# Kernel optimization log

Measured on AMD Instinct MI355X. Metric: run time of the kernel, lower is better.

The kernel has to match this reference:

```python
import jax, jax.numpy as jnp
import numpy as np

B, S, V, D = 64, 1024, 1024, 512


def setup_inputs() -> dict:
    key = jax.random.key(0)
    ks = jax.random.split(key, 18)
    sd = 1.0 / np.sqrt(D)
    return dict(
        map_memory=jnp.zeros((B, S, V), jnp.float32),
        step_memory=jnp.zeros((B, S, S), jnp.float32),
        evidence=jax.random.normal(ks[0], (B, D), jnp.float32),
        marker_id=jax.random.randint(ks[1], (B,), 0, 4, jnp.int32),
        source_idx=jax.random.randint(ks[2], (B,), 0, S, jnp.int32),
        source_mask=jax.random.randint(ks[3], (B,), 0, 2, jnp.int32).astype(bool),
        target_symbol_idx=jax.random.randint(ks[4], (B,), 0, S, jnp.int32),
        target_symbol_mask=jax.random.randint(ks[5], (B,), 0, 2, jnp.int32).astype(bool),
        target_value_idx=jax.random.randint(ks[6], (B,), 0, V, jnp.int32),
        target_value_mask=jax.random.randint(ks[7], (B,), 0, 2, jnp.int32).astype(bool),
        map_W1=jax.random.normal(ks[8], (D, D), jnp.float32) * sd,
        map_b1=jnp.zeros((D,), jnp.float32),
        map_W2=jax.random.normal(ks[9], (D, 1), jnp.float32) * sd,
        map_b2=jnp.zeros((1,), jnp.float32),
        step_W1=jax.random.normal(ks[10], (D, D), jnp.float32) * sd,
        step_b1=jnp.zeros((D,), jnp.float32),
        step_W2=jax.random.normal(ks[11], (D, 1), jnp.float32) * sd,
        step_b2=jnp.zeros((1,), jnp.float32),
    )


def _gain(x, W1, b1, W2, b2):
    # Dense -> gelu (flax default: approximate) -> Dense(1)
    h = jax.nn.gelu(x @ W1 + b1)
    return (h @ W2 + b2)[:, 0]  # [B]


def reference(map_memory, step_memory, evidence, marker_id, source_idx,
              source_mask, target_symbol_idx, target_symbol_mask,
              target_value_idx, target_value_mask,
              map_W1, map_b1, map_W2, map_b2,
              step_W1, step_b1, step_W2, step_b2):
    map_gate = jax.nn.sigmoid(_gain(evidence, map_W1, map_b1, map_W2, map_b2))    # [B]
    step_gate = jax.nn.sigmoid(_gain(evidence, step_W1, step_b1, step_W2, step_b2))  # [B]
    map_mask = ((marker_id == 1) | (marker_id == 2)) & source_mask & target_value_mask
    step_mask = (marker_id == 3) & source_mask & target_symbol_mask
    b = jnp.arange(map_memory.shape[0])
    # one-hot outer product 'bs,bv->bsv' * gate is exactly a single gated entry at
    # (source_idx, target_idx) per batch element -> indexed scatter-add.
    next_map = map_memory.at[b, source_idx, target_value_idx].add(
        map_gate * map_mask.astype(map_gate.dtype))
    next_step = step_memory.at[b, source_idx, target_symbol_idx].add(
        step_gate * step_mask.astype(step_gate.dtype))
    return next_map, next_step
```

## Files before the change

### kernel.cpp

```cpp
#include <hip/hip_runtime.h>
#include <math.h>

#define BB 64
#define SS 1024
#define VV 1024
#define DD 512

__device__ __forceinline__ float gelu_tanh(float x) {
    const float k = 0.7978845608028654f;
    float x3 = x * x * x;
    return 0.5f * x * (1.0f + tanhf(k * (x + 0.044715f * x3)));
}

__global__ void __launch_bounds__(256)
gate_scatter_kernel(
    const float* __restrict__ evidence,
    const int* __restrict__ marker_id,
    const int* __restrict__ source_idx,
    const int* __restrict__ source_mask,
    const int* __restrict__ target_symbol_idx,
    const int* __restrict__ target_symbol_mask,
    const int* __restrict__ target_value_idx,
    const int* __restrict__ target_value_mask,
    const float* __restrict__ map_W1, const float* __restrict__ map_b1,
    const float* __restrict__ map_W2, const float* __restrict__ map_b2,
    const float* __restrict__ step_W1, const float* __restrict__ step_b1,
    const float* __restrict__ step_W2, const float* __restrict__ step_b2,
    float* __restrict__ out)
{
    const int b    = blockIdx.x >> 1;
    const int head = blockIdx.x & 1;
    const float* W1  = head ? step_W1 : map_W1;
    const float* b1  = head ? step_b1 : map_b1;
    const float* W2  = head ? step_W2 : map_W2;
    const float* b2v = head ? step_b2 : map_b2;

    __shared__ float ev[DD];
    __shared__ float wsum[4];

    const int tid = threadIdx.x;
    for (int i = tid; i < DD; i += 256) ev[i] = evidence[b * DD + i];
    __syncthreads();

    float acc = 0.0f;
    #pragma unroll
    for (int jj = 0; jj < DD; jj += 256) {
        const int j = jj + tid;
        float h = b1[j];
        for (int k = 0; k < DD; ++k) {
            h = fmaf(ev[k], W1[k * DD + j], h);
        }
        h = gelu_tanh(h);
        acc = fmaf(h, W2[j], acc);
    }

    #pragma unroll
    for (int off = 32; off > 0; off >>= 1) acc += __shfl_down(acc, off, 64);
    if ((tid & 63) == 0) wsum[tid >> 6] = acc;
    __syncthreads();

    if (tid == 0) {
        float g = wsum[0] + wsum[1] + wsum[2] + wsum[3] + b2v[0];
        g = 1.0f / (1.0f + expf(-g));
        const int m  = marker_id[b];
        const bool sm = source_mask[b] != 0;
        if (head == 0) {
            const bool mask = ((m == 1) || (m == 2)) && sm && (target_value_mask[b] != 0);
            if (mask) {
                size_t idx = (size_t)b * SS * VV + (size_t)source_idx[b] * VV
                           + (size_t)target_value_idx[b];
                out[idx] += g;
            }
        } else {
            const bool mask = (m == 3) && sm && (target_symbol_mask[b] != 0);
            if (mask) {
                size_t idx = (size_t)BB * SS * VV + (size_t)b * SS * SS
                           + (size_t)source_idx[b] * SS + (size_t)target_symbol_idx[b];
                out[idx] += g;
            }
        }
    }
}

extern "C" void kernel_launch(void* const* d_in, const int* in_sizes, int n_in,
                              void* d_out, int out_size, void* d_ws, size_t ws_size,
                              hipStream_t stream) {
    const float* map_memory  = (const float*)d_in[0];
    const float* step_memory = (const float*)d_in[1];
    const float* evidence    = (const float*)d_in[2];
    const int* marker_id     = (const int*)d_in[3];
    const int* source_idx    = (const int*)d_in[4];
    const int* source_mask         = (const int*)d_in[5];
    const int* target_symbol_idx   = (const int*)d_in[6];
    const int* target_symbol_mask  = (const int*)d_in[7];
    const int* target_value_idx    = (const int*)d_in[8];
    const int* target_value_mask   = (const int*)d_in[9];
    const float* map_W1  = (const float*)d_in[10];
    const float* map_b1  = (const float*)d_in[11];
    const float* map_W2  = (const float*)d_in[12];
    const float* map_b2  = (const float*)d_in[13];
    const float* step_W1 = (const float*)d_in[14];
    const float* step_b1 = (const float*)d_in[15];
    const float* step_W2 = (const float*)d_in[16];
    const float* step_b2 = (const float*)d_in[17];

    float* out = (float*)d_out;
    const size_t map_elems  = (size_t)BB * SS * VV;
    const size_t step_elems = (size_t)BB * SS * SS;

    hipMemcpyAsync(out, map_memory, map_elems * sizeof(float),
                   hipMemcpyDeviceToDevice, stream);
    hipMemcpyAsync(out + map_elems, step_memory, step_elems * sizeof(float),
                   hipMemcpyDeviceToDevice, stream);

    dim3 grid(BB * 2);
    dim3 block(256);
    gate_scatter_kernel<<<grid, block, 0, stream>>>(
        evidence, marker_id, source_idx, source_mask,
        target_symbol_idx, target_symbol_mask,
        target_value_idx, target_value_mask,
        map_W1, map_b1, map_W2, map_b2,
        step_W1, step_b1, step_W2, step_b2,
        out);
}
```

Baseline: 246.7 us.

## Fuse memory copy with gated scatter into a single vectorized copy kernel

Replaces the two device-to-device memcpys and the separate scatter kernel with a gate kernel that writes scatter indices and gate values to workspace, followed by a float4 copy kernel that applies matching updates while streaming the memory. This removes the read-modify-write tail and the memcpy launch overhead, and lets the copy be a custom kernel. It adds an extra pass over the index list in every copy block, and the int indices stay close to the 32-bit range.

Result: slower. 253.0 us (+2.5%).

```diff
diff --git a/kernel.cpp b/kernel.cpp
--- a/kernel.cpp
+++ b/kernel.cpp
@@ -6,6 +6,15 @@
 #define VV 1024
 #define DD 512
 
+#define MAP_WORDS  ((size_t)BB * SS * VV)
+#define STEP_WORDS ((size_t)BB * SS * SS)
+#define TOT_WORDS  (MAP_WORDS + STEP_WORDS)
+#define TOT_F4     (TOT_WORDS / 4)
+#define MAP_F4     (MAP_WORDS / 4)
+#define COPY_BLOCKS 8192
+#define F4_PER_BLOCK (TOT_F4 / COPY_BLOCKS)
+#define NGATES (BB * 2)
+
 __device__ __forceinline__ float gelu_tanh(float x) {
     const float k = 0.7978845608028654f;
     float x3 = x * x * x;
@@ -13,7 +22,7 @@
 }
 
 __global__ void __launch_bounds__(256)
-gate_scatter_kernel(
+gate_kernel(
     const float* __restrict__ evidence,
     const int* __restrict__ marker_id,
     const int* __restrict__ source_idx,
@@ -26,7 +35,7 @@
     const float* __restrict__ map_W2, const float* __restrict__ map_b2,
     const float* __restrict__ step_W1, const float* __restrict__ step_b1,
     const float* __restrict__ step_W2, const float* __restrict__ step_b2,
-    float* __restrict__ out)
+    int* __restrict__ ws_idx, float* __restrict__ ws_g)
 {
     const int b    = blockIdx.x >> 1;
     const int head = blockIdx.x & 1;
@@ -64,21 +73,75 @@
         g = 1.0f / (1.0f + expf(-g));
         const int m  = marker_id[b];
         const bool sm = source_mask[b] != 0;
+        int idx = -1;
         if (head == 0) {
-            const bool mask = ((m == 1) || (m == 2)) && sm && (target_value_mask[b] != 0);
-            if (mask) {
-                size_t idx = (size_t)b * SS * VV + (size_t)source_idx[b] * VV
-                           + (size_t)target_value_idx[b];
-                out[idx] += g;
+            if (((m == 1) || (m == 2)) && sm && (target_value_mask[b] != 0)) {
+                idx = b * (SS * VV) + source_idx[b] * VV + target_value_idx[b];
             }
         } else {
-            const bool mask = (m == 3) && sm && (target_symbol_mask[b] != 0);
-            if (mask) {
-                size_t idx = (size_t)BB * SS * VV + (size_t)b * SS * SS
-                           + (size_t)source_idx[b] * SS + (size_t)target_symbol_idx[b];
-                out[idx] += g;
+            if ((m == 3) && sm && (target_symbol_mask[b] != 0)) {
+                idx = (int)MAP_WORDS + b * (SS * SS) + source_idx[b] * SS
+                    + target_symbol_idx[b];
             }
         }
+        ws_idx[blockIdx.x] = idx;
+        ws_g[blockIdx.x]   = g;
+    }
+}
+
+__global__ void __launch_bounds__(256)
+copy_scatter_kernel(
+    const float4* __restrict__ map_memory,
+    const float4* __restrict__ step_memory,
+    const int* __restrict__ ws_idx,
+    const float* __restrict__ ws_g,
+    float4* __restrict__ out)
+{
+    const long f4_base = (long)blockIdx.x * F4_PER_BLOCK;
+
+    __shared__ int n_match;
+    __shared__ int m_f4[8];
+    __shared__ int m_lane[8];
+    __shared__ float m_g[8];
+
+    if (threadIdx.x == 0) n_match = 0;
+    __syncthreads();
+    if (threadIdx.x < NGATES) {
+        int idx = ws_idx[threadIdx.x];
+        if (idx >= 0) {
+            long f4 = (long)(idx >> 2);
+            long off = f4 - f4_base;
+            if (off >= 0 && off < F4_PER_BLOCK) {
+                int slot = atomicAdd(&n_match, 1);
+                m_f4[slot]   = (int)off;
+                m_lane[slot] = idx & 3;
+                m_g[slot]    = ws_g[threadIdx.x];
+            }
+        }
+    }
+    __syncthreads();
+    const int nm = n_match;
+
+    const float4* __restrict__ src =
+        (f4_base < (long)MAP_F4) ? (map_memory + f4_base)
+                                 : (step_memory + (f4_base - (long)MAP_F4));
+    float4* __restrict__ dst = out + f4_base;
+
+    for (int i = threadIdx.x; i < F4_PER_BLOCK; i += 256) {
+        float4 v = src[i];
+        if (nm) {
+            for (int e = 0; e < nm; ++e) {
+                if (m_f4[e] == i) {
+                    const int ln = m_lane[e];
+                    const float g = m_g[e];
+                    v.x += (ln == 0) ? g : 0.0f;
+                    v.y += (ln == 1) ? g : 0.0f;
+                    v.z += (ln == 2) ? g : 0.0f;
+                    v.w += (ln == 3) ? g : 0.0f;
+                }
+            }
+        }
+        dst[i] = v;
     }
 }
 
@@ -90,11 +153,11 @@
     const float* evidence    = (const float*)d_in[2];
     const int* marker_id     = (const int*)d_in[3];
     const int* source_idx    = (const int*)d_in[4];
-    const int* source_mask         = (const int*)d_in[5];
-    const int* target_symbol_idx   = (const int*)d_in[6];
-    const int* target_symbol_mask  = (const int*)d_in[7];
-    const int* target_value_idx    = (const int*)d_in[8];
-    const int* target_value_mask   = (const int*)d_in[9];
+    const int* source_mask        = (const int*)d_in[5];
+    const int* target_symbol_idx  = (const int*)d_in[6];
+    const int* target_symbol_mask = (const int*)d_in[7];
+    const int* target_value_idx   = (const int*)d_in[8];
+    const int* target_value_mask  = (const int*)d_in[9];
     const float* map_W1  = (const float*)d_in[10];
     const float* map_b1  = (const float*)d_in[11];
     const float* map_W2  = (const float*)d_in[12];
@@ -104,22 +167,19 @@
     const float* step_W2 = (const float*)d_in[16];
     const float* step_b2 = (const float*)d_in[17];
 
-    float* out = (float*)d_out;
-    const size_t map_elems  = (size_t)BB * SS * VV;
-    const size_t step_elems = (size_t)BB * SS * SS;
+    char* ws = (char*)d_ws;
+    int*   ws_idx = (int*)ws;
+    float* ws_g   = (float*)(ws + NGATES * sizeof(int));
 
-    hipMemcpyAsync(out, map_memory, map_elems * sizeof(float),
-                   hipMemcpyDeviceToDevice, stream);
-    hipMemcpyAsync(out + map_elems, step_memory, step_elems * sizeof(float),
-                   hipMemcpyDeviceToDevice, stream);
-
-    dim3 grid(BB * 2);
-    dim3 block(256);
-    gate_scatter_kernel<<<grid, block, 0, stream>>>(
+    gate_kernel<<<dim3(NGATES), dim3(256), 0, stream>>>(
         evidence, marker_id, source_idx, source_mask,
         target_symbol_idx, target_symbol_mask,
         target_value_idx, target_value_mask,
         map_W1, map_b1, map_W2, map_b2,
         step_W1, step_b1, step_W2, step_b2,
-        out);
+        ws_idx, ws_g);
+
+    copy_scatter_kernel<<<dim3(COPY_BLOCKS), dim3(256), 0, stream>>>(
+        (const float4*)map_memory, (const float4*)step_memory,
+        ws_idx, ws_g, (float4*)d_out);
 }
```
